# Kernel tuning notes

Measured on AMD Instinct MI355X. Metric: run time of the kernel, lower is better.

Reference implementation:

```python
import jax, jax.numpy as jnp
import numpy as np
import math

D_MODEL = 1024
NUM_HEADS = 16
D_HEAD = D_MODEL // NUM_HEADS


def setup_inputs() -> dict:
    key = jax.random.key(0)
    k1, k2, k3, k4, k5 = jax.random.split(key, 5)
    scale = 1.0 / math.sqrt(D_MODEL)
    x = jax.random.normal(k1, (4, 2048, D_MODEL), dtype=jnp.float32)
    W_qkv = jax.random.normal(k2, (D_MODEL, 3 * D_MODEL), dtype=jnp.float32) * scale
    b_qkv = jax.random.normal(k3, (3 * D_MODEL,), dtype=jnp.float32) * 0.02
    W_o = jax.random.normal(k4, (D_MODEL, D_MODEL), dtype=jnp.float32) * scale
    b_o = jax.random.normal(k5, (D_MODEL,), dtype=jnp.float32) * 0.02
    return {"x": x, "W_qkv": W_qkv, "b_qkv": b_qkv, "W_o": W_o, "b_o": b_o}


def reference(x, W_qkv, b_qkv, W_o, b_o):
    B, C, D = x.shape
    H, Dh = NUM_HEADS, D_HEAD
    qkv = x @ W_qkv + b_qkv                       # [B, C, 3D]
    qkv = qkv.reshape(B, C, 3, H, Dh).transpose(2, 0, 3, 1, 4)  # [3, B, H, C, Dh]
    Q, K, V = qkv[0], qkv[1], qkv[2]
    scores = jnp.einsum('bhqd,bhkd->bhqk', Q, K) / math.sqrt(Dh)  # [B, H, C, C]
    causal = jnp.tril(jnp.ones((C, C), dtype=bool))
    scores = jnp.where(causal, scores, -jnp.inf)
    weights = jax.nn.softmax(scores, axis=-1)
    attn = jnp.einsum('bhqk,bhkd->bhqd', weights, V)              # [B, H, C, Dh]
    attn = attn.transpose(0, 2, 1, 3).reshape(B, C, D)
    return attn @ W_o + b_o
```

## Files before the change

kernel.cpp:

```cpp
#include <hip/hip_runtime.h>
#include <hip/hip_bf16.h>
#include <stdint.h>


typedef __attribute__((ext_vector_type(8))) short short8;
typedef __attribute__((ext_vector_type(4))) short short4v;
typedef __attribute__((ext_vector_type(4))) float f32x4;

#define AS1 __attribute__((address_space(1)))
#define AS3 __attribute__((address_space(3)))

static __device__ __forceinline__ short f2bf(float f) {
  union { float f; uint32_t u; } v; v.f = f;
  uint32_t r = v.u + 0x7fffu + ((v.u >> 16) & 1u);
  return (short)(r >> 16);
}

static __device__ __forceinline__ short f2bfh(float f) {
  __hip_bfloat16 h = __float2bfloat16(f);
  return *reinterpret_cast<short*>(&h);
}

static __device__ __forceinline__ void gload_lds16(const void* g, void* l) {
  __builtin_amdgcn_global_load_lds((const AS1 void*)g, (AS3 void*)l, 16, 0, 0);
}

#define MFMA16(a, b, c) __builtin_amdgcn_mfma_f32_16x16x32_bf16((a), (b), (c), 0, 0, 0)

__global__ __launch_bounds__(256) void k_cvt_x(const float* __restrict__ x,
                                               short* __restrict__ xb) {
  long i = ((long)blockIdx.x * 256 + threadIdx.x) * 4;
  const float4 v = *(const float4*)(x + i);
  short4v o;
  o[0] = f2bf(v.x); o[1] = f2bf(v.y); o[2] = f2bf(v.z); o[3] = f2bf(v.w);
  *(short4v*)(xb + i) = o;
}

__global__ __launch_bounds__(256) void k_transpose_bf(const float* __restrict__ W,
                                                      short* __restrict__ Wt,
                                                      int K, int N) {
  __shared__ float t[64][65];
  const int nb = blockIdx.x * 64, kb = blockIdx.y * 64;
  const int tid = threadIdx.x;
#pragma unroll
  for (int i = 0; i < 16; ++i) {
    int idx = i * 256 + tid; int r = idx >> 6, c = idx & 63;
    t[r][c] = W[(long)(kb + r) * N + nb + c];
  }
  __syncthreads();
#pragma unroll
  for (int i = 0; i < 16; ++i) {
    int idx = i * 256 + tid; int r = idx >> 6, c = idx & 63;
    Wt[(long)(nb + r) * K + kb + c] = f2bf(t[c][r]);
  }
}

template <int EPI>
__global__ __launch_bounds__(512, 2)
void k_gemm(const short* __restrict__ A, const short* __restrict__ Bt,
            const float* __restrict__ bias, float* __restrict__ Cf,
            short* __restrict__ q_ws, short* __restrict__ k_ws, short* __restrict__ vt_ws,
            int M, int N, int K) {
  __shared__ __align__(16) short a_sh[3][128 * 64];
  __shared__ __align__(16) short b_sh[3][256 * 64];
  const int tid = threadIdx.x;
  const int lane = tid & 63, wid = tid >> 6;
  const int l15 = lane & 15, lg = lane >> 4;
  const int s7 = l15 & 7;
  const int wgm = wid >> 2, wgn = wid & 3;

  const int nbx = (EPI == 0) ? 12 : 4;
  const int id = blockIdx.x;
  const int cpx = (nbx * 64) >> 3;
  const int nid = (id & 7) * cpx + (id >> 3);
  const int m0 = (nid / nbx) * 128, n0 = (nid % nbx) * 256;

  f32x4 acc[2][4][2] = {};

  const int srow = tid >> 3, sgr = tid & 7;

#define STAGE_A(buf, kb, j)                                                          \
  {                                                                                  \
    int row = (j) * 64 + srow;                                                       \
    gload_lds16(A + (long)(m0 + row) * K + (kb) + ((sgr ^ (row & 7)) << 3),          \
                &a_sh[buf][((j) * 512 + tid) * 8]);                                  \
  }
#define STAGE_B(buf, kb, j)                                                          \
  {                                                                                  \
    int row = (j) * 64 + srow;                                                       \
    gload_lds16(Bt + (long)(n0 + row) * K + (kb) + ((sgr ^ (row & 7)) << 3),         \
                &b_sh[buf][((j) * 512 + tid) * 8]);                                  \
  }
#define STAGE6(buf, kb)                                                              \
  {                                                                                  \
    STAGE_A(buf, kb, 0); STAGE_A(buf, kb, 1);                                        \
    STAGE_B(buf, kb, 0); STAGE_B(buf, kb, 1); STAGE_B(buf, kb, 2); STAGE_B(buf, kb, 3); \
  }

  STAGE6(0, 0);
  STAGE6(1, 64);
  asm volatile("s_waitcnt vmcnt(6)" ::: "memory");
  __builtin_amdgcn_sched_barrier(0);
  __builtin_amdgcn_s_barrier();

  const int nt = K >> 6;
  int rd = 0;
  for (int t = 0; t < nt; ++t) {
    const int wr = (rd >= 1) ? rd - 1 : rd + 2;
    const int kb2 = (t + 2) << 6;
    const bool pre = (t + 2 < nt);

    short8 af[4][2], bf[2][2];
#pragma unroll
    for (int mi = 0; mi < 4; ++mi)
#pragma unroll
      for (int kk = 0; kk < 2; ++kk) {
        const int row = (wgm * 4 + mi) * 16 + l15;
        af[mi][kk] = *(const short8*)(&a_sh[rd][row * 64 + (((kk * 4 + lg) ^ s7) << 3)]);
      }
#pragma unroll
    for (int ni = 0; ni < 2; ++ni)
#pragma unroll
      for (int kk = 0; kk < 2; ++kk) {
        const int row = (wgn * 2 + ni) * 16 + l15;
        bf[ni][kk] = *(const short8*)(&b_sh[rd][row * 64 + (((kk * 4 + lg) ^ s7) << 3)]);
      }
    if (pre) { STAGE_A(wr, kb2, 0); STAGE_A(wr, kb2, 1); STAGE_B(wr, kb2, 0); }
    __builtin_amdgcn_s_setprio(1);
#pragma unroll
    for (int mi = 0; mi < 4; ++mi)
#pragma unroll
      for (int ni = 0; ni < 2; ++ni)
#pragma unroll
        for (int kk = 0; kk < 2; ++kk)
          acc[0][mi][ni] = MFMA16(af[mi][kk], bf[ni][kk], acc[0][mi][ni]);
    __builtin_amdgcn_s_setprio(0);

    short8 bg[2][2];
#pragma unroll
    for (int ni = 0; ni < 2; ++ni)
#pragma unroll
      for (int kk = 0; kk < 2; ++kk) {
        const int row = 128 + (wgn * 2 + ni) * 16 + l15;
        bg[ni][kk] = *(const short8*)(&b_sh[rd][row * 64 + (((kk * 4 + lg) ^ s7) << 3)]);
      }
    if (pre) { STAGE_B(wr, kb2, 1); STAGE_B(wr, kb2, 2); STAGE_B(wr, kb2, 3); }
    __builtin_amdgcn_s_setprio(1);
#pragma unroll
    for (int mi = 0; mi < 4; ++mi)
#pragma unroll
      for (int ni = 0; ni < 2; ++ni)
#pragma unroll
        for (int kk = 0; kk < 2; ++kk)
          acc[1][mi][ni] = MFMA16(af[mi][kk], bg[ni][kk], acc[1][mi][ni]);
    __builtin_amdgcn_s_setprio(0);

    if (pre) asm volatile("s_waitcnt vmcnt(6)" ::: "memory");
    else     asm volatile("s_waitcnt vmcnt(0)" ::: "memory");
    __builtin_amdgcn_sched_barrier(0);
    __builtin_amdgcn_s_barrier();
    __builtin_amdgcn_sched_barrier(0);
    rd = (rd == 2) ? 0 : rd + 1;
  }
#undef STAGE_A
#undef STAGE_B
#undef STAGE6

#pragma unroll
  for (int h = 0; h < 2; ++h) {
#pragma unroll
    for (int mi = 0; mi < 4; ++mi) {
#pragma unroll
      for (int ni = 0; ni < 2; ++ni) {
        const int n = n0 + h * 128 + (wgn * 2 + ni) * 16 + l15;
        const int mb = m0 + (wgm * 4 + mi) * 16 + lg * 4;
        if (EPI == 1) {
#pragma unroll
          for (int r = 0; r < 4; ++r)
            Cf[(long)(mb + r) * N + n] = acc[h][mi][ni][r] + bias[n];
        } else {
          const int which = n >> 10;
          const int hh = (n >> 6) & 15, d = n & 63;
          const int b = mb >> 11, c = mb & 2047;
          const int bh = b * 16 + hh;
          const float bi = bias[n];
          if (which == 2) {
            short4v o;
#pragma unroll
            for (int r = 0; r < 4; ++r) o[r] = f2bf(acc[h][mi][ni][r] + bi);
            *(short4v*)(vt_ws + ((long)bh * 64 + d) * 2048 + c) = o;
          } else if (which == 0) {
#pragma unroll
            for (int r = 0; r < 4; ++r)
              q_ws[((long)bh * 2048 + c + r) * 64 + d] = f2bf((acc[h][mi][ni][r] + bi) * 0.18033688011f);
          } else {
#pragma unroll
            for (int r = 0; r < 4; ++r)
              k_ws[((long)bh * 2048 + c + r) * 64 + d] = f2bf(acc[h][mi][ni][r] + bi);
          }
        }
      }
    }
  }
}

__global__ __launch_bounds__(128)
void k_attn(const short* __restrict__ q_ws, const short* __restrict__ k_ws,
            const short* __restrict__ vt_ws, short* __restrict__ attn_out) {
  __shared__ __align__(16) short k_sh[2][64 * 64];
  __shared__ __align__(16) short v_sh[2][64 * 64];

  const int tid = threadIdx.x;
  const int lane = tid & 63, wid = tid >> 6;
  const int l15 = lane & 15, lg = lane >> 4;
  const int bh = blockIdx.x;
  const int qt = (int)gridDim.y - 1 - (int)blockIdx.y;
  const int b = bh >> 4, h = bh & 15;
  const int qwA = qt * 64 + wid * 16;
  const int qwB = qwA + 32;
  const int qA = qwA + l15, qB = qwB + l15;
  const int nt = qt + 1;

  const short* qrowA = q_ws + ((long)bh * 2048 + qA) * 64;
  const short* qrowB = q_ws + ((long)bh * 2048 + qB) * 64;
  const short8 qfA0 = *(const short8*)(qrowA + lg * 8);
  const short8 qfA1 = *(const short8*)(qrowA + 32 + lg * 8);
  const short8 qfB0 = *(const short8*)(qrowB + lg * 8);
  const short8 qfB1 = *(const short8*)(qrowB + 32 + lg * 8);

  const int s7 = l15 & 7;
  const int koff0 = ((lg ^ s7) << 4);
  const int koff1 = (((4 + lg) ^ s7) << 4);
  const int vsub = (lg & 1) * 8, vg = lg >> 1;
  int voff[4];
#pragma unroll
  for (int m2 = 0; m2 < 4; ++m2)
    voff[m2] = (((2 * m2 + vg) ^ s7) << 4) | vsub;

  f32x4 accA[4] = {}, accB[4] = {};
  float lA = 0.f, lB = 0.f;

  const int srow = tid >> 3, sg = tid & 7;

#define STAGE(buf, kv)                                                              \
  {                                                                                 \
    _Pragma("unroll")                                                               \
    for (int i = 0; i < 4; ++i) {                                                   \
      int row = i * 16 + srow;                                                      \
      int gl = sg ^ (row & 7);                                                      \
      gload_lds16(k_ws + ((long)bh * 2048 + (kv) + row) * 64 + gl * 8,              \
                  &k_sh[buf][(i * 128 + tid) * 8]);                                 \
      gload_lds16(vt_ws + ((long)bh * 64 + row) * 2048 + (kv) + gl * 8,             \
                  &v_sh[buf][(i * 128 + tid) * 8]);                                 \
    }                                                                               \
  }

  STAGE(0, 0);
  asm volatile("s_waitcnt vmcnt(0)" ::: "memory");
  __syncthreads();

  int cur = 0;
  for (int t = 0; t < nt; ++t) {
    const int kv0 = t * 64;
    if (t + 1 < nt) STAGE(cur ^ 1, kv0 + 64);

    const char* ksh = (const char*)k_sh[cur];
    const char* vsh = (const char*)v_sh[cur];

    f32x4 stA[4], stB[4];
    __builtin_amdgcn_s_setprio(1);
#pragma unroll
    for (int j = 0; j < 4; ++j) {
      const char* kr = ksh + (j * 16 + l15) * 128;
      short8 kf0 = *(const short8*)(kr + koff0);
      short8 kf1 = *(const short8*)(kr + koff1);
      f32x4 zA = {};
      zA = MFMA16(kf0, qfA0, zA);
      zA = MFMA16(kf1, qfA1, zA);
      stA[j] = zA;
      f32x4 zB = {};
      zB = MFMA16(kf0, qfB0, zB);
      zB = MFMA16(kf1, qfB1, zB);
      stB[j] = zB;
    }
    __builtin_amdgcn_s_setprio(0);

    if (t == nt - 1) {
#pragma unroll
      for (int j = 0; j < 4; ++j) {
        int kvr = kv0 + j * 16 + lg * 4;
#pragma unroll
        for (int r = 0; r < 4; ++r) {
          if (kvr + r > qA) stA[j][r] = -1e30f;
          if (kvr + r > qB) stB[j][r] = -1e30f;
        }
      }
    }

    short8 pA0, pA1, pB0, pB1;
    {
      float ps = 0.f;
#pragma unroll
      for (int j = 0; j < 4; ++j)
#pragma unroll
        for (int r = 0; r < 4; ++r) {
          float e = __builtin_amdgcn_exp2f(stA[j][r]);
          stA[j][r] = e;
          ps += e;
        }
      lA += ps;
#pragma unroll
      for (int r = 0; r < 4; ++r) {
        pA0[r]     = f2bfh(stA[0][r]);
        pA0[4 + r] = f2bfh(stA[1][r]);
        pA1[r]     = f2bfh(stA[2][r]);
        pA1[4 + r] = f2bfh(stA[3][r]);
      }
    }
    {
      float ps = 0.f;
#pragma unroll
      for (int j = 0; j < 4; ++j)
#pragma unroll
        for (int r = 0; r < 4; ++r) {
          float e = __builtin_amdgcn_exp2f(stB[j][r]);
          stB[j][r] = e;
          ps += e;
        }
      lB += ps;
#pragma unroll
      for (int r = 0; r < 4; ++r) {
        pB0[r]     = f2bfh(stB[0][r]);
        pB0[4 + r] = f2bfh(stB[1][r]);
        pB1[r]     = f2bfh(stB[2][r]);
        pB1[4 + r] = f2bfh(stB[3][r]);
      }
    }

    __builtin_amdgcn_s_setprio(1);
#pragma unroll
    for (int dt = 0; dt < 4; ++dt) {
      const char* vr = vsh + (dt * 16 + l15) * 128;
      union { short8 s8; short4v s4[2]; } vf1, vf2;
      vf1.s4[0] = *(const short4v*)(vr + voff[0]);
      vf1.s4[1] = *(const short4v*)(vr + voff[1]);
      vf2.s4[0] = *(const short4v*)(vr + voff[2]);
      vf2.s4[1] = *(const short4v*)(vr + voff[3]);
      accA[dt] = MFMA16(vf1.s8, pA0, accA[dt]);
      accA[dt] = MFMA16(vf2.s8, pA1, accA[dt]);
      accB[dt] = MFMA16(vf1.s8, pB0, accB[dt]);
      accB[dt] = MFMA16(vf2.s8, pB1, accB[dt]);
    }
    __builtin_amdgcn_s_setprio(0);

    asm volatile("s_waitcnt vmcnt(0)" ::: "memory");
    __syncthreads();
    cur ^= 1;
  }
#undef STAGE

  {
    float lt = lA;
    lt += __shfl_xor(lt, 16);
    lt += __shfl_xor(lt, 32);
    const float inv = 1.0f / lt;
    short* obase = attn_out + ((long)b * 2048 + qA) * 1024 + h * 64;
#pragma unroll
    for (int dt = 0; dt < 4; ++dt) {
      short4v o;
#pragma unroll
      for (int r = 0; r < 4; ++r) o[r] = f2bfh(accA[dt][r] * inv);
      *(short4v*)(obase + dt * 16 + lg * 4) = o;
    }
  }
  {
    float lt = lB;
    lt += __shfl_xor(lt, 16);
    lt += __shfl_xor(lt, 32);
    const float inv = 1.0f / lt;
    short* obase = attn_out + ((long)b * 2048 + qB) * 1024 + h * 64;
#pragma unroll
    for (int dt = 0; dt < 4; ++dt) {
      short4v o;
#pragma unroll
      for (int r = 0; r < 4; ++r) o[r] = f2bfh(accB[dt][r] * inv);
      *(short4v*)(obase + dt * 16 + lg * 4) = o;
    }
  }
}

extern "C" void kernel_launch(void* const* d_in, const int* in_sizes, int n_in,
                              void* d_out, int out_size, void* d_ws, size_t ws_size,
                              hipStream_t stream) {
  const float* x     = (const float*)d_in[0];
  const float* W_qkv = (const float*)d_in[1];
  const float* b_qkv = (const float*)d_in[2];
  const float* W_o   = (const float*)d_in[3];
  const float* b_o   = (const float*)d_in[4];
  float* out = (float*)d_out;

  char* ws = (char*)d_ws;
  short* x_bf   = (short*)(ws);
  short* wqkv_t = (short*)(ws + 16777216);
  short* wo_t   = (short*)(ws + 23068672);
  short* q_ws   = (short*)(ws + 25165824);
  short* k_ws   = (short*)(ws + 41943040);
  short* vt_ws  = (short*)(ws + 58720256);

  k_cvt_x<<<dim3(8192), dim3(256), 0, stream>>>(x, x_bf);
  k_transpose_bf<<<dim3(48, 16), dim3(256), 0, stream>>>(W_qkv, wqkv_t, 1024, 3072);
  k_transpose_bf<<<dim3(16, 16), dim3(256), 0, stream>>>(W_o, wo_t, 1024, 1024);
  k_gemm<0><<<dim3(768), dim3(512), 0, stream>>>(x_bf, wqkv_t, b_qkv, nullptr,
                                                 q_ws, k_ws, vt_ws, 8192, 3072, 1024);
  k_attn<<<dim3(64, 32), dim3(128), 0, stream>>>(q_ws, k_ws, vt_ws, x_bf);
  k_gemm<1><<<dim3(256), dim3(512), 0, stream>>>(x_bf, wo_t, b_o, out,
                                                 nullptr, nullptr, nullptr, 8192, 1024, 1024);
}
```

Baseline: 161.8 us.

## Load K and V fragments directly from global memory, dropping LDS double buffering

The attention kernel no longer stages K and V tiles into swizzled shared-memory double buffers with async global-to-LDS loads. Each lane now reads its MFMA operand fragments straight from global memory (through cache), which removes the LDS traffic and the per-tile barrier and waitcnt. In exchange it loses explicit prefetch overlap and cross-wave reuse, so the two waves load the same K/V data twice and exposed global latency may stall the MFMAs.

```diff
diff --git a/kernel.cpp b/kernel.cpp
--- a/kernel.cpp
+++ b/kernel.cpp
@@ -207,9 +207,6 @@
 __global__ __launch_bounds__(128)
 void k_attn(const short* __restrict__ q_ws, const short* __restrict__ k_ws,
             const short* __restrict__ vt_ws, short* __restrict__ attn_out) {
-  __shared__ __align__(16) short k_sh[2][64 * 64];
-  __shared__ __align__(16) short v_sh[2][64 * 64];
-
   const int tid = threadIdx.x;
   const int lane = tid & 63, wid = tid >> 6;
   const int l15 = lane & 15, lg = lane >> 4;
@@ -228,52 +225,23 @@
   const short8 qfB0 = *(const short8*)(qrowB + lg * 8);
   const short8 qfB1 = *(const short8*)(qrowB + 32 + lg * 8);
 
-  const int s7 = l15 & 7;
-  const int koff0 = ((lg ^ s7) << 4);
-  const int koff1 = (((4 + lg) ^ s7) << 4);
-  const int vsub = (lg & 1) * 8, vg = lg >> 1;
-  int voff[4];
-#pragma unroll
-  for (int m2 = 0; m2 < 4; ++m2)
-    voff[m2] = (((2 * m2 + vg) ^ s7) << 4) | vsub;
+  const short* kbase = k_ws + ((long)bh * 2048 + l15) * 64;
+  const short* vbase = vt_ws + ((long)bh * 64 + l15) * 2048;
+  const int vg = lg >> 1, ve = (lg & 1) * 4;
 
   f32x4 accA[4] = {}, accB[4] = {};
   float lA = 0.f, lB = 0.f;
 
-  const int srow = tid >> 3, sg = tid & 7;
-
-#define STAGE(buf, kv)                                                              \
-  {                                                                                 \
-    _Pragma("unroll")                                                               \
-    for (int i = 0; i < 4; ++i) {                                                   \
-      int row = i * 16 + srow;                                                      \
-      int gl = sg ^ (row & 7);                                                      \
-      gload_lds16(k_ws + ((long)bh * 2048 + (kv) + row) * 64 + gl * 8,              \
-                  &k_sh[buf][(i * 128 + tid) * 8]);                                 \
-      gload_lds16(vt_ws + ((long)bh * 64 + row) * 2048 + (kv) + gl * 8,             \
-                  &v_sh[buf][(i * 128 + tid) * 8]);                                 \
-    }                                                                               \
-  }
-
-  STAGE(0, 0);
-  asm volatile("s_waitcnt vmcnt(0)" ::: "memory");
-  __syncthreads();
-
-  int cur = 0;
   for (int t = 0; t < nt; ++t) {
     const int kv0 = t * 64;
-    if (t + 1 < nt) STAGE(cur ^ 1, kv0 + 64);
-
-    const char* ksh = (const char*)k_sh[cur];
-    const char* vsh = (const char*)v_sh[cur];
 
     f32x4 stA[4], stB[4];
     __builtin_amdgcn_s_setprio(1);
 #pragma unroll
     for (int j = 0; j < 4; ++j) {
-      const char* kr = ksh + (j * 16 + l15) * 128;
-      short8 kf0 = *(const short8*)(kr + koff0);
-      short8 kf1 = *(const short8*)(kr + koff1);
+      const short* kr = kbase + (long)(kv0 + j * 16) * 64;
+      short8 kf0 = *(const short8*)(kr + lg * 8);
+      short8 kf1 = *(const short8*)(kr + 32 + lg * 8);
       f32x4 zA = {};
       zA = MFMA16(kf0, qfA0, zA);
       zA = MFMA16(kf1, qfA1, zA);
@@ -340,24 +308,19 @@
     __builtin_amdgcn_s_setprio(1);
 #pragma unroll
     for (int dt = 0; dt < 4; ++dt) {
-      const char* vr = vsh + (dt * 16 + l15) * 128;
+      const short* vr = vbase + (long)dt * 16 * 2048 + kv0 + ve;
       union { short8 s8; short4v s4[2]; } vf1, vf2;
-      vf1.s4[0] = *(const short4v*)(vr + voff[0]);
-      vf1.s4[1] = *(const short4v*)(vr + voff[1]);
-      vf2.s4[0] = *(const short4v*)(vr + voff[2]);
-      vf2.s4[1] = *(const short4v*)(vr + voff[3]);
+      vf1.s4[0] = *(const short4v*)(vr + (2 * 0 + vg) * 8);
+      vf1.s4[1] = *(const short4v*)(vr + (2 * 1 + vg) * 8);
+      vf2.s4[0] = *(const short4v*)(vr + (2 * 2 + vg) * 8);
+      vf2.s4[1] = *(const short4v*)(vr + (2 * 3 + vg) * 8);
       accA[dt] = MFMA16(vf1.s8, pA0, accA[dt]);
       accA[dt] = MFMA16(vf2.s8, pA1, accA[dt]);
       accB[dt] = MFMA16(vf1.s8, pB0, accB[dt]);
       accB[dt] = MFMA16(vf2.s8, pB1, accB[dt]);
     }
     __builtin_amdgcn_s_setprio(0);
-
-    asm volatile("s_waitcnt vmcnt(0)" ::: "memory");
-    __syncthreads();
-    cur ^= 1;
-  }
-#undef STAGE
+  }
 
   {
     float lt = lA;
```

After: 290.3 us. 79.5% more time.
